# Optimization experiments

Measured on AMD Instinct MI355X. Metric: run time of the kernel, lower is better.

The kernel has to match this reference:

```python
import jax, jax.numpy as jnp
import numpy as np

B, F, CHUNK = 4096, 1024, 128  # batch, features, scan chunk size
EPS = 1e-5  # nn.LayerNorm default eps


def setup_inputs() -> dict:
    key = jax.random.key(0)
    k1, k2 = jax.random.split(key, 2)
    x = jax.random.normal(k1, (B, F), dtype=jnp.float32)
    W = jax.random.normal(k2, (F, F), dtype=jnp.float32) * 0.5  # init_weight = randn*0.5
    b = jnp.zeros((F,), dtype=jnp.float32)
    gamma = jnp.ones((F,), dtype=jnp.float32)   # LayerNorm weight
    beta = jnp.zeros((F,), dtype=jnp.float32)   # LayerNorm bias
    return {"x": x, "W": W, "b": b, "gamma": gamma, "beta": beta}


def reference(x, W, b, gamma, beta):
    # LayerNorm over last dim (biased variance, as torch)
    mu = jnp.mean(x, axis=-1, keepdims=True)
    var = jnp.mean(jnp.square(x - mu), axis=-1, keepdims=True)
    xn = (x - mu) * jax.lax.rsqrt(var + EPS) * gamma + beta  # [B, F]

    # Tropical max-plus matmul: out[b, i] = max_k xn[b, k] + W[k, i]
    # Chunk the batch to avoid materializing the full [B, F, F] broadcast-add.
    xc = xn.reshape(B // CHUNK, CHUNK, F)

    def step(_, xb):  # xb: [CHUNK, F]
        o = jnp.max(xb[:, :, None] + W[None, :, :], axis=1)  # [CHUNK, F]
        return None, o

    _, out = jax.lax.scan(step, None, xc)
    out = out.reshape(B, F)

    # Tropical bias: elementwise max with learned threshold b
    return jnp.maximum(out, b)
```

## Files before the change

### kernel.cpp

```cpp
#include <hip/hip_runtime.h>
#include <math.h>

#define F 1024
#define BM 128
#define BN 128
#define BK 16

typedef _Float16 h2 __attribute__((ext_vector_type(2)));
typedef _Float16 h4 __attribute__((ext_vector_type(4)));
typedef _Float16 h8 __attribute__((ext_vector_type(8)));
typedef float v4f __attribute__((ext_vector_type(4)));

static __device__ __forceinline__ float fmax3(float a, float b, float c) {
  float d;
  asm("v_max3_f32 %0, %1, %2, %3" : "=v"(d) : "v"(a), "v"(b), "v"(c));
  return d;
}
static __device__ __forceinline__ h2 pk_max(h2 a, h2 b) {
  h2 d;
  asm("v_pk_max_f16 %0, %1, %2" : "=v"(d) : "v"(a), "v"(b));
  return d;
}

__global__ __launch_bounds__(256) void ln_kernel(const float* __restrict__ x,
                                                 const float* __restrict__ gamma,
                                                 const float* __restrict__ beta,
                                                 float* __restrict__ xn) {
  const int lane = threadIdx.x & 63;
  const int wv = threadIdx.x >> 6;
  const int row = blockIdx.x * 4 + wv;
  const float4* xr = (const float4*)(x + (size_t)row * F);
  float4 v[4];
  float s = 0.f;
#pragma unroll
  for (int j = 0; j < 4; ++j) {
    v[j] = xr[lane + 64 * j];
    s += v[j].x + v[j].y + v[j].z + v[j].w;
  }
#pragma unroll
  for (int off = 32; off; off >>= 1) s += __shfl_xor(s, off, 64);
  const float mu = s * (1.0f / F);
  float sq = 0.f;
#pragma unroll
  for (int j = 0; j < 4; ++j) {
    v[j].x -= mu; v[j].y -= mu; v[j].z -= mu; v[j].w -= mu;
    sq += v[j].x * v[j].x + v[j].y * v[j].y + v[j].z * v[j].z + v[j].w * v[j].w;
  }
#pragma unroll
  for (int off = 32; off; off >>= 1) sq += __shfl_xor(sq, off, 64);
  const float r = rsqrtf(sq * (1.0f / F) + 1e-5f);
  const float4* g4 = (const float4*)gamma;
  const float4* b4 = (const float4*)beta;
  float4* o = (float4*)(xn + (size_t)row * F);
#pragma unroll
  for (int j = 0; j < 4; ++j) {
    const int idx = lane + 64 * j;
    const float4 g = g4[idx];
    const float4 bb = b4[idx];
    float4 ov;
    ov.x = v[j].x * r * g.x + bb.x;
    ov.y = v[j].y * r * g.y + bb.y;
    ov.z = v[j].z * r * g.z + bb.z;
    ov.w = v[j].w * r * g.w + bb.w;
    o[idx] = ov;
  }
}

__global__ __launch_bounds__(256, 4) void trop_f(const float* __restrict__ A,
                                                 const float* __restrict__ Wm,
                                                 const float* __restrict__ bias,
                                                 _Float16* __restrict__ dsth,
                                                 float* __restrict__ outf,
                                                 int ntiles, int totrows, int fuse) {
  __shared__ float As[2][BK][BM + 4];
  __shared__ float Bs[2][BK][BN];

  const int tid = threadIdx.x;
  const int tx = tid & 15;
  const int ty = tid >> 4;
  const int row0 = blockIdx.y * BM;
  const int col0 = blockIdx.x * BN;
  const int kbase = blockIdx.z * ntiles * BK;

  const int am = tid >> 2;
  const int ak = (tid & 3) << 2;
  const int bk = tid >> 5;
  const int bn = (tid & 31) << 2;

  const float* Arow0 = A + (size_t)(row0 + am) * F + kbase + ak;
  const float* Arow1 = A + (size_t)(row0 + am + 64) * F + kbase + ak;
  const float* Wrow0 = Wm + (size_t)(kbase + bk) * F + col0 + bn;
  const float* Wrow1 = Wm + (size_t)(kbase + bk + 8) * F + col0 + bn;

  float acc[8][8];
#pragma unroll
  for (int m = 0; m < 8; ++m)
#pragma unroll
    for (int n = 0; n < 8; ++n) acc[m][n] = -INFINITY;

  {
    const float4 a0s = *(const float4*)(Arow0);
    const float4 a1s = *(const float4*)(Arow1);
    const float4 b0s = *(const float4*)(Wrow0);
    const float4 b1s = *(const float4*)(Wrow1);
    As[0][ak + 0][am] = a0s.x;
    As[0][ak + 1][am] = a0s.y;
    As[0][ak + 2][am] = a0s.z;
    As[0][ak + 3][am] = a0s.w;
    As[0][ak + 0][am + 64] = a1s.x;
    As[0][ak + 1][am + 64] = a1s.y;
    As[0][ak + 2][am + 64] = a1s.z;
    As[0][ak + 3][am + 64] = a1s.w;
    *(float4*)&Bs[0][bk][bn] = b0s;
    *(float4*)&Bs[0][bk + 8][bn] = b1s;
  }
  __syncthreads();

  for (int kt = 0; kt < ntiles; ++kt) {
    const int cur = kt & 1;
    float4 a0s, a1s, b0s, b1s;
    if (kt + 1 < ntiles) {
      const int k0 = (kt + 1) * BK;
      a0s = *(const float4*)(Arow0 + k0);
      a1s = *(const float4*)(Arow1 + k0);
      b0s = *(const float4*)(Wrow0 + (size_t)k0 * F);
      b1s = *(const float4*)(Wrow1 + (size_t)k0 * F);
    }

#pragma unroll
    for (int k = 0; k < BK; k += 2) {
      float a0[8], a1[8];
      *(float4*)&a0[0] = *(const float4*)&As[cur][k][ty * 8];
      *(float4*)&a0[4] = *(const float4*)&As[cur][k][ty * 8 + 4];
      *(float4*)&a1[0] = *(const float4*)&As[cur][k + 1][ty * 8];
      *(float4*)&a1[4] = *(const float4*)&As[cur][k + 1][ty * 8 + 4];
#pragma unroll
      for (int h = 0; h < 2; ++h) {
        float b0[4], b1[4];
        *(float4*)&b0[0] = *(const float4*)&Bs[cur][k][h * 64 + tx * 4];
        *(float4*)&b1[0] = *(const float4*)&Bs[cur][k + 1][h * 64 + tx * 4];
#pragma unroll
        for (int m = 0; m < 8; ++m)
#pragma unroll
          for (int n = 0; n < 4; ++n) {
            const float t0 = a0[m] + b0[n];
            const float t1 = a1[m] + b1[n];
            acc[m][h * 4 + n] = fmax3(acc[m][h * 4 + n], t0, t1);
          }
      }
    }

    if (kt + 1 < ntiles) {
      const int nxt = cur ^ 1;
      As[nxt][ak + 0][am] = a0s.x;
      As[nxt][ak + 1][am] = a0s.y;
      As[nxt][ak + 2][am] = a0s.z;
      As[nxt][ak + 3][am] = a0s.w;
      As[nxt][ak + 0][am + 64] = a1s.x;
      As[nxt][ak + 1][am + 64] = a1s.y;
      As[nxt][ak + 2][am + 64] = a1s.z;
      As[nxt][ak + 3][am + 64] = a1s.w;
      *(float4*)&Bs[nxt][bk][bn] = b0s;
      *(float4*)&Bs[nxt][bk + 8][bn] = b1s;
      __syncthreads();
    }
  }

  if (fuse) {
    const float4 bv0 = *(const float4*)(bias + col0 + tx * 4);
    const float4 bv1 = *(const float4*)(bias + col0 + 64 + tx * 4);
#pragma unroll
    for (int m = 0; m < 8; ++m) {
      float* orow = outf + (size_t)(row0 + ty * 8 + m) * F + col0 + tx * 4;
      float4 o0, o1;
      o0.x = fmaxf(acc[m][0], bv0.x);
      o0.y = fmaxf(acc[m][1], bv0.y);
      o0.z = fmaxf(acc[m][2], bv0.z);
      o0.w = fmaxf(acc[m][3], bv0.w);
      o1.x = fmaxf(acc[m][4], bv1.x);
      o1.y = fmaxf(acc[m][5], bv1.y);
      o1.z = fmaxf(acc[m][6], bv1.z);
      o1.w = fmaxf(acc[m][7], bv1.w);
      *(float4*)orow = o0;
      *(float4*)(orow + 64) = o1;
    }
  } else {
    _Float16* base = dsth + (size_t)blockIdx.z * totrows * F;
#pragma unroll
    for (int m = 0; m < 8; ++m) {
      _Float16* orow = base + (size_t)(row0 + ty * 8 + m) * F + col0 + tx * 4;
      h4 o0 = {(_Float16)acc[m][0], (_Float16)acc[m][1],
               (_Float16)acc[m][2], (_Float16)acc[m][3]};
      h4 o1 = {(_Float16)acc[m][4], (_Float16)acc[m][5],
               (_Float16)acc[m][6], (_Float16)acc[m][7]};
      *(h4*)orow = o0;
      *(h4*)(orow + 64) = o1;
    }
  }
}

template <int NP>
__global__ __launch_bounds__(256) void combineNh(const _Float16* __restrict__ p,
                                                 size_t plane,
                                                 const float* __restrict__ bias,
                                                 float* __restrict__ out) {
  const int i = blockIdx.x * 256 + threadIdx.x;
  h8 v = ((const h8*)p)[i];
  h2* vv = (h2*)&v;
#pragma unroll
  for (int q = 1; q < NP; ++q) {
    const h8 u = ((const h8*)(p + (size_t)q * plane))[i];
    const h2* uu = (const h2*)&u;
#pragma unroll
    for (int j = 0; j < 4; ++j) vv[j] = pk_max(vv[j], uu[j]);
  }
  const int nb = (i & (F / 8 - 1)) * 8;
  const v4f bb0 = *(const v4f*)(bias + nb);
  const v4f bb1 = *(const v4f*)(bias + nb + 4);
  float4* o4 = (float4*)(out + (size_t)i * 8);
  float4 o0, o1;
  o0.x = fmaxf((float)v[0], bb0.x);
  o0.y = fmaxf((float)v[1], bb0.y);
  o0.z = fmaxf((float)v[2], bb0.z);
  o0.w = fmaxf((float)v[3], bb0.w);
  o1.x = fmaxf((float)v[4], bb1.x);
  o1.y = fmaxf((float)v[5], bb1.y);
  o1.z = fmaxf((float)v[6], bb1.z);
  o1.w = fmaxf((float)v[7], bb1.w);
  o4[0] = o0;
  o4[1] = o1;
}

extern "C" void kernel_launch(void* const* d_in, const int* in_sizes, int n_in,
                              void* d_out, int out_size, void* d_ws, size_t ws_size,
                              hipStream_t stream) {
  const float* x = (const float*)d_in[0];
  const float* Wm = (const float*)d_in[1];
  const float* bias = (const float*)d_in[2];
  const float* gamma = (const float*)d_in[3];
  const float* beta = (const float*)d_in[4];
  float* out = (float*)d_out;

  const int Brows = in_sizes[0] / F;
  const size_t plane = (size_t)Brows * F;

  float* xn = (float*)d_ws;
  _Float16* parts = (_Float16*)(xn + plane);

  ln_kernel<<<Brows / 4, 256, 0, stream>>>(x, gamma, beta, xn);

  const size_t need4 = plane * sizeof(float) + 4 * plane * sizeof(_Float16);
  const size_t need1 = plane * sizeof(float);
  if (ws_size >= need4) {
    dim3 grid(F / BN, Brows / BM, 4);
    trop_f<<<grid, 256, 0, stream>>>(xn, Wm, bias, parts, nullptr,
                                     (F / BK) / 4, Brows, 0);
    combineNh<4><<<(int)(plane / 2048), 256, 0, stream>>>(parts, plane, bias, out);
  } else if (ws_size >= need1) {
    dim3 grid(F / BN, Brows / BM, 1);
    trop_f<<<grid, 256, 0, stream>>>(xn, Wm, bias, nullptr, out, F / BK, Brows, 1);
  }
}
```

Measured before the change: 213.5 us.

## Quantize tropical matmul to packed int16 fixed-point with v_pk_add/max_i16

Converts the LayerNorm output and the weights to int16 fixed-point (scale 1024) and runs the max-plus product with packed i16 add and max instructions, two lanes per VALU op. A new kernel converts W on every call, and shared memory tiles shrink to shorts. The packed ops are meant to roughly halve VALU work and cut memory and LDS traffic. In exchange, values are clamped and quantized to about 1e-3 resolution, a loss of accuracy against the fp32 reference.

```diff
diff --git a/kernel.cpp b/kernel.cpp
--- a/kernel.cpp
+++ b/kernel.cpp
@@ -6,26 +6,38 @@
 #define BN 128
 #define BK 16
 
-typedef _Float16 h2 __attribute__((ext_vector_type(2)));
-typedef _Float16 h4 __attribute__((ext_vector_type(4)));
-typedef _Float16 h8 __attribute__((ext_vector_type(8)));
+typedef short s2 __attribute__((ext_vector_type(2)));
+typedef short s4 __attribute__((ext_vector_type(4)));
+typedef short s8 __attribute__((ext_vector_type(8)));
 typedef float v4f __attribute__((ext_vector_type(4)));
 
-static __device__ __forceinline__ float fmax3(float a, float b, float c) {
-  float d;
-  asm("v_max3_f32 %0, %1, %2, %3" : "=v"(d) : "v"(a), "v"(b), "v"(c));
+#define SCALE 1024.0f
+#define ISCALE (1.0f / 1024.0f)
+
+static __device__ __forceinline__ s2 pk_max_i16(s2 a, s2 b) {
+  s2 d;
+  asm("v_pk_max_i16 %0, %1, %2" : "=v"(d) : "v"(a), "v"(b));
   return d;
 }
-static __device__ __forceinline__ h2 pk_max(h2 a, h2 b) {
-  h2 d;
-  asm("v_pk_max_f16 %0, %1, %2" : "=v"(d) : "v"(a), "v"(b));
+static __device__ __forceinline__ s2 pk_add_blo(s2 a, s2 b) {
+  s2 d;
+  asm("v_pk_add_i16 %0, %1, %2 op_sel:[0,0] op_sel_hi:[0,1]" : "=v"(d) : "v"(a), "v"(b));
   return d;
+}
+static __device__ __forceinline__ s2 pk_add_bhi(s2 a, s2 b) {
+  s2 d;
+  asm("v_pk_add_i16 %0, %1, %2 op_sel:[1,0] op_sel_hi:[1,1]" : "=v"(d) : "v"(a), "v"(b));
+  return d;
+}
+
+static __device__ __forceinline__ short q_i16(float v, float clampv) {
+  return (short)__float2int_rn(fminf(fmaxf(v * SCALE, -clampv), clampv));
 }
 
 __global__ __launch_bounds__(256) void ln_kernel(const float* __restrict__ x,
                                                  const float* __restrict__ gamma,
                                                  const float* __restrict__ beta,
-                                                 float* __restrict__ xn) {
+                                                 short* __restrict__ xn) {
   const int lane = threadIdx.x & 63;
   const int wv = threadIdx.x >> 6;
   const int row = blockIdx.x * 4 + wv;
@@ -51,29 +63,41 @@
   const float r = rsqrtf(sq * (1.0f / F) + 1e-5f);
   const float4* g4 = (const float4*)gamma;
   const float4* b4 = (const float4*)beta;
-  float4* o = (float4*)(xn + (size_t)row * F);
+  s4* o = (s4*)(xn + (size_t)row * F);
 #pragma unroll
   for (int j = 0; j < 4; ++j) {
     const int idx = lane + 64 * j;
     const float4 g = g4[idx];
     const float4 bb = b4[idx];
-    float4 ov;
-    ov.x = v[j].x * r * g.x + bb.x;
-    ov.y = v[j].y * r * g.y + bb.y;
-    ov.z = v[j].z * r * g.z + bb.z;
-    ov.w = v[j].w * r * g.w + bb.w;
-    o[idx] = ov;
-  }
-}
-
-__global__ __launch_bounds__(256, 4) void trop_f(const float* __restrict__ A,
-                                                 const float* __restrict__ Wm,
+    s4 q;
+    q[0] = q_i16(v[j].x * r * g.x + bb.x, 28000.f);
+    q[1] = q_i16(v[j].y * r * g.y + bb.y, 28000.f);
+    q[2] = q_i16(v[j].z * r * g.z + bb.z, 28000.f);
+    q[3] = q_i16(v[j].w * r * g.w + bb.w, 28000.f);
+    o[idx] = q;
+  }
+}
+
+__global__ __launch_bounds__(256) void cvt_kernel(const float* __restrict__ Wf,
+                                                  short* __restrict__ Wq) {
+  const int i = blockIdx.x * 256 + threadIdx.x;
+  const float4 v = ((const float4*)Wf)[i];
+  s4 q;
+  q[0] = q_i16(v.x, 4700.f);
+  q[1] = q_i16(v.y, 4700.f);
+  q[2] = q_i16(v.z, 4700.f);
+  q[3] = q_i16(v.w, 4700.f);
+  ((s4*)Wq)[i] = q;
+}
+
+__global__ __launch_bounds__(256, 4) void trop_i(const short* __restrict__ A,
+                                                 const short* __restrict__ Wm,
                                                  const float* __restrict__ bias,
-                                                 _Float16* __restrict__ dsth,
+                                                 short* __restrict__ dsts,
                                                  float* __restrict__ outf,
                                                  int ntiles, int totrows, int fuse) {
-  __shared__ float As[2][BK][BM + 4];
-  __shared__ float Bs[2][BK][BN];
+  __shared__ alignas(16) short As[2][BK][BM];
+  __shared__ alignas(16) short Bs[2][BK][BN];
 
   const int tid = threadIdx.x;
   const int tx = tid & 15;
@@ -82,151 +106,126 @@
   const int col0 = blockIdx.x * BN;
   const int kbase = blockIdx.z * ntiles * BK;
 
-  const int am = tid >> 2;
-  const int ak = (tid & 3) << 2;
-  const int bk = tid >> 5;
-  const int bn = (tid & 31) << 2;
-
-  const float* Arow0 = A + (size_t)(row0 + am) * F + kbase + ak;
-  const float* Arow1 = A + (size_t)(row0 + am + 64) * F + kbase + ak;
-  const float* Wrow0 = Wm + (size_t)(kbase + bk) * F + col0 + bn;
-  const float* Wrow1 = Wm + (size_t)(kbase + bk + 8) * F + col0 + bn;
-
-  float acc[8][8];
+  const int ar = tid & 127;
+  const int ak = (tid >> 7) << 3;
+  const int bk = tid >> 4;
+  const int bn = (tid & 15) << 3;
+
+  const short* Arow = A + (size_t)(row0 + ar) * F + kbase + ak;
+  const short* Wrow = Wm + (size_t)(kbase + bk) * F + col0 + bn;
+
+  s2 acc[8][4];
+  const s2 ninf = {(short)-32768, (short)-32768};
 #pragma unroll
   for (int m = 0; m < 8; ++m)
 #pragma unroll
-    for (int n = 0; n < 8; ++n) acc[m][n] = -INFINITY;
+    for (int n = 0; n < 4; ++n) acc[m][n] = ninf;
 
   {
-    const float4 a0s = *(const float4*)(Arow0);
-    const float4 a1s = *(const float4*)(Arow1);
-    const float4 b0s = *(const float4*)(Wrow0);
-    const float4 b1s = *(const float4*)(Wrow1);
-    As[0][ak + 0][am] = a0s.x;
-    As[0][ak + 1][am] = a0s.y;
-    As[0][ak + 2][am] = a0s.z;
-    As[0][ak + 3][am] = a0s.w;
-    As[0][ak + 0][am + 64] = a1s.x;
-    As[0][ak + 1][am + 64] = a1s.y;
-    As[0][ak + 2][am + 64] = a1s.z;
-    As[0][ak + 3][am + 64] = a1s.w;
-    *(float4*)&Bs[0][bk][bn] = b0s;
-    *(float4*)&Bs[0][bk + 8][bn] = b1s;
+    const s8 av = *(const s8*)Arow;
+    const s8 bv = *(const s8*)Wrow;
+#pragma unroll
+    for (int j = 0; j < 8; ++j) As[0][ak + j][ar] = av[j];
+    *(s8*)&Bs[0][bk][bn] = bv;
   }
   __syncthreads();
 
   for (int kt = 0; kt < ntiles; ++kt) {
     const int cur = kt & 1;
-    float4 a0s, a1s, b0s, b1s;
+    s8 av, bv;
     if (kt + 1 < ntiles) {
-      const int k0 = (kt + 1) * BK;
-      a0s = *(const float4*)(Arow0 + k0);
-      a1s = *(const float4*)(Arow1 + k0);
-      b0s = *(const float4*)(Wrow0 + (size_t)k0 * F);
-      b1s = *(const float4*)(Wrow1 + (size_t)k0 * F);
-    }
-
-#pragma unroll
-    for (int k = 0; k < BK; k += 2) {
-      float a0[8], a1[8];
-      *(float4*)&a0[0] = *(const float4*)&As[cur][k][ty * 8];
-      *(float4*)&a0[4] = *(const float4*)&As[cur][k][ty * 8 + 4];
-      *(float4*)&a1[0] = *(const float4*)&As[cur][k + 1][ty * 8];
-      *(float4*)&a1[4] = *(const float4*)&As[cur][k + 1][ty * 8 + 4];
-#pragma unroll
-      for (int h = 0; h < 2; ++h) {
-        float b0[4], b1[4];
-        *(float4*)&b0[0] = *(const float4*)&Bs[cur][k][h * 64 + tx * 4];
-        *(float4*)&b1[0] = *(const float4*)&Bs[cur][k + 1][h * 64 + tx * 4];
-#pragma unroll
-        for (int m = 0; m < 8; ++m)
-#pragma unroll
-          for (int n = 0; n < 4; ++n) {
-            const float t0 = a0[m] + b0[n];
-            const float t1 = a1[m] + b1[n];
-            acc[m][h * 4 + n] = fmax3(acc[m][h * 4 + n], t0, t1);
-          }
+      av = *(const s8*)(Arow + (kt + 1) * BK);
+      bv = *(const s8*)(Wrow + (size_t)(kt + 1) * BK * F);
+    }
+
+#pragma unroll
+    for (int k = 0; k < BK; ++k) {
+      s8 a = *(const s8*)&As[cur][k][ty * 8];
+      s8 b = *(const s8*)&Bs[cur][k][tx * 8];
+      const s2* a2 = (const s2*)&a;
+      const s2* b2 = (const s2*)&b;
+#pragma unroll
+      for (int m = 0; m < 8; ++m) {
+        const s2 am = a2[m >> 1];
+#pragma unroll
+        for (int nn = 0; nn < 4; ++nn) {
+          const s2 t = (m & 1) ? pk_add_bhi(am, b2[nn]) : pk_add_blo(am, b2[nn]);
+          acc[m][nn] = pk_max_i16(acc[m][nn], t);
+        }
       }
     }
 
     if (kt + 1 < ntiles) {
       const int nxt = cur ^ 1;
-      As[nxt][ak + 0][am] = a0s.x;
-      As[nxt][ak + 1][am] = a0s.y;
-      As[nxt][ak + 2][am] = a0s.z;
-      As[nxt][ak + 3][am] = a0s.w;
-      As[nxt][ak + 0][am + 64] = a1s.x;
-      As[nxt][ak + 1][am + 64] = a1s.y;
-      As[nxt][ak + 2][am + 64] = a1s.z;
-      As[nxt][ak + 3][am + 64] = a1s.w;
-      *(float4*)&Bs[nxt][bk][bn] = b0s;
-      *(float4*)&Bs[nxt][bk + 8][bn] = b1s;
+#pragma unroll
+      for (int j = 0; j < 8; ++j) As[nxt][ak + j][ar] = av[j];
+      *(s8*)&Bs[nxt][bk][bn] = bv;
       __syncthreads();
     }
   }
 
   if (fuse) {
-    const float4 bv0 = *(const float4*)(bias + col0 + tx * 4);
-    const float4 bv1 = *(const float4*)(bias + col0 + 64 + tx * 4);
+    const float4 bv0 = *(const float4*)(bias + col0 + tx * 8);
+    const float4 bv1 = *(const float4*)(bias + col0 + tx * 8 + 4);
 #pragma unroll
     for (int m = 0; m < 8; ++m) {
-      float* orow = outf + (size_t)(row0 + ty * 8 + m) * F + col0 + tx * 4;
+      float* orow = outf + (size_t)(row0 + ty * 8 + m) * F + col0 + tx * 8;
       float4 o0, o1;
-      o0.x = fmaxf(acc[m][0], bv0.x);
-      o0.y = fmaxf(acc[m][1], bv0.y);
-      o0.z = fmaxf(acc[m][2], bv0.z);
-      o0.w = fmaxf(acc[m][3], bv0.w);
-      o1.x = fmaxf(acc[m][4], bv1.x);
-      o1.y = fmaxf(acc[m][5], bv1.y);
-      o1.z = fmaxf(acc[m][6], bv1.z);
-      o1.w = fmaxf(acc[m][7], bv1.w);
+      o0.x = fmaxf((float)acc[m][0][0] * ISCALE, bv0.x);
+      o0.y = fmaxf((float)acc[m][0][1] * ISCALE, bv0.y);
+      o0.z = fmaxf((float)acc[m][1][0] * ISCALE, bv0.z);
+      o0.w = fmaxf((float)acc[m][1][1] * ISCALE, bv0.w);
+      o1.x = fmaxf((float)acc[m][2][0] * ISCALE, bv1.x);
+      o1.y = fmaxf((float)acc[m][2][1] * ISCALE, bv1.y);
+      o1.z = fmaxf((float)acc[m][3][0] * ISCALE, bv1.z);
+      o1.w = fmaxf((float)acc[m][3][1] * ISCALE, bv1.w);
       *(float4*)orow = o0;
-      *(float4*)(orow + 64) = o1;
+      *(float4*)(orow + 4) = o1;
     }
   } else {
-    _Float16* base = dsth + (size_t)blockIdx.z * totrows * F;
+    short* base = dsts + (size_t)blockIdx.z * totrows * F;
 #pragma unroll
     for (int m = 0; m < 8; ++m) {
-      _Float16* orow = base + (size_t)(row0 + ty * 8 + m) * F + col0 + tx * 4;
-      h4 o0 = {(_Float16)acc[m][0], (_Float16)acc[m][1],
-               (_Float16)acc[m][2], (_Float16)acc[m][3]};
-      h4 o1 = {(_Float16)acc[m][4], (_Float16)acc[m][5],
-               (_Float16)acc[m][6], (_Float16)acc[m][7]};
-      *(h4*)orow = o0;
-      *(h4*)(orow + 64) = o1;
+      short* orow = base + (size_t)(row0 + ty * 8 + m) * F + col0 + tx * 8;
+      s8 o;
+#pragma unroll
+      for (int nn = 0; nn < 4; ++nn) {
+        o[2 * nn] = acc[m][nn][0];
+        o[2 * nn + 1] = acc[m][nn][1];
+      }
+      *(s8*)orow = o;
     }
   }
 }
 
 template <int NP>
-__global__ __launch_bounds__(256) void combineNh(const _Float16* __restrict__ p,
+__global__ __launch_bounds__(256) void combineNs(const short* __restrict__ p,
                                                  size_t plane,
                                                  const float* __restrict__ bias,
                                                  float* __restrict__ out) {
   const int i = blockIdx.x * 256 + threadIdx.x;
-  h8 v = ((const h8*)p)[i];
-  h2* vv = (h2*)&v;
+  s8 v = ((const s8*)p)[i];
+  s2* vv = (s2*)&v;
 #pragma unroll
   for (int q = 1; q < NP; ++q) {
-    const h8 u = ((const h8*)(p + (size_t)q * plane))[i];
-    const h2* uu = (const h2*)&u;
-#pragma unroll
-    for (int j = 0; j < 4; ++j) vv[j] = pk_max(vv[j], uu[j]);
+    const s8 u = ((const s8*)(p + (size_t)q * plane))[i];
+    const s2* uu = (const s2*)&u;
+#pragma unroll
+    for (int j = 0; j < 4; ++j) vv[j] = pk_max_i16(vv[j], uu[j]);
   }
   const int nb = (i & (F / 8 - 1)) * 8;
   const v4f bb0 = *(const v4f*)(bias + nb);
   const v4f bb1 = *(const v4f*)(bias + nb + 4);
   float4* o4 = (float4*)(out + (size_t)i * 8);
   float4 o0, o1;
-  o0.x = fmaxf((float)v[0], bb0.x);
-  o0.y = fmaxf((float)v[1], bb0.y);
-  o0.z = fmaxf((float)v[2], bb0.z);
-  o0.w = fmaxf((float)v[3], bb0.w);
-  o1.x = fmaxf((float)v[4], bb1.x);
-  o1.y = fmaxf((float)v[5], bb1.y);
-  o1.z = fmaxf((float)v[6], bb1.z);
-  o1.w = fmaxf((float)v[7], bb1.w);
+  o0.x = fmaxf((float)v[0] * ISCALE, bb0.x);
+  o0.y = fmaxf((float)v[1] * ISCALE, bb0.y);
+  o0.z = fmaxf((float)v[2] * ISCALE, bb0.z);
+  o0.w = fmaxf((float)v[3] * ISCALE, bb0.w);
+  o1.x = fmaxf((float)v[4] * ISCALE, bb1.x);
+  o1.y = fmaxf((float)v[5] * ISCALE, bb1.y);
+  o1.z = fmaxf((float)v[6] * ISCALE, bb1.z);
+  o1.w = fmaxf((float)v[7] * ISCALE, bb1.w);
   o4[0] = o0;
   o4[1] = o1;
 }
@@ -244,20 +243,22 @@
   const int Brows = in_sizes[0] / F;
   const size_t plane = (size_t)Brows * F;
 
-  float* xn = (float*)d_ws;
-  _Float16* parts = (_Float16*)(xn + plane);
-
-  ln_kernel<<<Brows / 4, 256, 0, stream>>>(x, gamma, beta, xn);
-
-  const size_t need4 = plane * sizeof(float) + 4 * plane * sizeof(_Float16);
-  const size_t need1 = plane * sizeof(float);
+  short* xnq = (short*)d_ws;
+  short* Wq = xnq + plane;
+  short* parts = Wq + (size_t)F * F;
+
+  ln_kernel<<<Brows / 4, 256, 0, stream>>>(x, gamma, beta, xnq);
+  cvt_kernel<<<(F * F) / 1024, 256, 0, stream>>>(Wm, Wq);
+
+  const size_t need4 = plane * 2 + (size_t)F * F * 2 + 4 * plane * 2;
+  const size_t need1 = plane * 2 + (size_t)F * F * 2;
   if (ws_size >= need4) {
     dim3 grid(F / BN, Brows / BM, 4);
-    trop_f<<<grid, 256, 0, stream>>>(xn, Wm, bias, parts, nullptr,
+    trop_i<<<grid, 256, 0, stream>>>(xnq, Wq, bias, parts, nullptr,
                                      (F / BK) / 4, Brows, 0);
-    combineNh<4><<<(int)(plane / 2048), 256, 0, stream>>>(parts, plane, bias, out);
+    combineNs<4><<<(int)(plane / 2048), 256, 0, stream>>>(parts, plane, bias, out);
   } else if (ws_size >= need1) {
     dim3 grid(F / BN, Brows / BM, 1);
-    trop_f<<<grid, 256, 0, stream>>>(xn, Wm, bias, nullptr, out, F / BK, Brows, 1);
-  }
-}
+    trop_i<<<grid, 256, 0, stream>>>(xnq, Wq, bias, nullptr, out, F / BK, Brows, 1);
+  }
+}
```

Measured after the change: 223.3 us. 4.6% more time.
